# Performance work log

Measured on AMD Instinct MI355X. Metric: run time of the kernel, lower is better.

The kernel has to match this reference:

```python
import jax, jax.numpy as jnp
import numpy as np

B, T, N, L, D, F = 8, 1024, 512, 4096, 512, 64  # batch, target, nodes, leaves, d_model, d_feature
BR = L // N  # branching factor: leaves per node


def setup_inputs() -> dict:
    key = jax.random.key(0)
    ks = jax.random.split(key, 10)
    s = 0.02
    return {
        "root": jax.random.normal(ks[0], (B, 1, F), dtype=jnp.float32),
        "node": jax.random.normal(ks[1], (B, N, D), dtype=jnp.float32),
        "leaf": jax.random.normal(ks[2], (B, L, D), dtype=jnp.float32),
        "target": jax.random.normal(ks[3], (B, T, D), dtype=jnp.float32),
        "Wq": jax.random.normal(ks[4], (D, F), dtype=jnp.float32) * s,
        "bq": jnp.zeros((F,), dtype=jnp.float32),
        "Wk": jax.random.normal(ks[5], (D, F), dtype=jnp.float32) * s,
        "bk": jnp.zeros((F,), dtype=jnp.float32),
        "Wv": jax.random.normal(ks[6], (D, F), dtype=jnp.float32) * s,
        "bv": jnp.zeros((F,), dtype=jnp.float32),
        "Wagg": jax.random.normal(ks[7], (D, 1), dtype=jnp.float32) * s,
        "bagg": jnp.zeros((1,), dtype=jnp.float32),
    }


def reference(root, node, leaf, target, Wq, bq, Wk, bk, Wv, bv, Wagg, bagg):
    # Shared DecoderLinear projections (same weights used for node and leaf).
    q = target @ Wq + bq                      # [B,T,F]
    node_k = node @ Wk + bk                   # [B,N,F]
    node_v = node @ Wv + bv                   # [B,N,F]
    leaf_k = leaf @ Wk + bk                   # [B,L,F]
    leaf_v = leaf @ Wv + bv                   # [B,L,F]

    scale = 1.0 / jnp.sqrt(jnp.asarray(F, dtype=q.dtype))
    # Dual-key attention weights (no value-matmul inside attention()).
    Aqn = jax.nn.softmax(jnp.einsum('btf,bnf->btn', q, node_k) * scale, axis=-1)  # [B,T,N]
    Aql = jax.nn.softmax(jnp.einsum('btf,blf->btl', q, leaf_k) * scale, axis=-1)  # [B,T,L]

    # Tree interpolation: each leaf mixes root, its parent node value, and itself.
    node_rep = jnp.repeat(node_v, BR, axis=1)               # [B,L,F]
    interp = (root + node_rep + leaf_v) / 3.0               # [B,L,F]

    # Upward cumulative aggregation: suffix mean along the leaf dimension.
    rev_cumsum = jnp.cumsum(interp[:, ::-1, :], axis=1)[:, ::-1, :]  # [B,L,F]
    counts = (L - jnp.arange(L)).astype(interp.dtype)[None, :, None]
    upward = rev_cumsum / counts                                     # [B,L,F]

    # Weighted aggregation: learned softmax weights over each node's leaf group.
    w = jax.nn.softmax((leaf @ Wagg + bagg).reshape(B, N, BR), axis=-1)   # [B,N,BR]
    node_hat = jnp.einsum('bnc,bncf->bnf', w, upward.reshape(B, N, BR, F))  # [B,N,F]

    # Fused cat + matmul + softmax.
    A = jnp.concatenate([Aqn, Aql], axis=-1)          # [B,T,N+L]
    V = jnp.concatenate([node_hat, leaf_v], axis=-2)  # [B,N+L,F]
    return jax.nn.softmax(jnp.einsum('btm,bmf->btf', A, V), axis=-1)  # [B,T,F]
```

## Files before the change

kernel.cpp:

```cpp
#include <hip/hip_runtime.h>

#define B_ 8
#define T_ 1024
#define N_ 512
#define L_ 4096
#define D_ 512
#define F_ 64
#define SLICES 8
#define TPS 9
#define KSTR 72
#define XSTR 520

typedef __attribute__((ext_vector_type(8))) short short8;
typedef __attribute__((ext_vector_type(4))) float f32x4;

__device__ __forceinline__ unsigned short f2bf(float x){
    unsigned u = __builtin_bit_cast(unsigned, x);
    u += 0x7FFFu + ((u >> 16) & 1u);
    return (unsigned short)(u >> 16);
}
__device__ __forceinline__ unsigned pack_bf(float lo, float hi){
    return (unsigned)f2bf(lo) | ((unsigned)f2bf(hi) << 16);
}
__device__ __forceinline__ float bf2f(unsigned short s){
    return __builtin_bit_cast(float, ((unsigned)s) << 16);
}
__device__ __forceinline__ short8 frag_from4(unsigned d0, unsigned d1, unsigned d2, unsigned d3){
    union { unsigned u[4]; short8 s; } t;
    t.u[0] = d0; t.u[1] = d1; t.u[2] = d2; t.u[3] = d3;
    return t.s;
}

__global__ __launch_bounds__(64)
void prep_kernel(const float* __restrict__ Wq, const float* __restrict__ bq,
                 const float* __restrict__ Wk, const float* __restrict__ bk,
                 const float* __restrict__ Wv, const float* __restrict__ bv,
                 unsigned short* __restrict__ Wq_t, unsigned short* __restrict__ Wkv_t,
                 float* __restrict__ bq_s, float* __restrict__ bkv)
{
    const int n = blockIdx.x;
    const int lane = threadIdx.x;
    if (n == 192) {
        bq_s[lane]   = bq[lane] * 0.125f;
        bkv[lane]    = bk[lane];
        bkv[64+lane] = bv[lane];
        return;
    }
    const int d0 = lane * 8;
    unsigned short t[8];
    if (n < 64) {
        #pragma unroll
        for (int j = 0; j < 8; ++j) t[j] = f2bf(Wq[(size_t)(d0+j)*F_ + n] * 0.125f);
        *(uint4*)&Wq_t[(size_t)n*D_ + d0] = make_uint4(
            (unsigned)t[0]|((unsigned)t[1]<<16), (unsigned)t[2]|((unsigned)t[3]<<16),
            (unsigned)t[4]|((unsigned)t[5]<<16), (unsigned)t[6]|((unsigned)t[7]<<16));
    } else {
        const int nn  = n - 64;
        const float* W = (nn < 64) ? Wk : Wv;
        const int col = nn & 63;
        #pragma unroll
        for (int j = 0; j < 8; ++j) t[j] = f2bf(W[(size_t)(d0+j)*F_ + col]);
        *(uint4*)&Wkv_t[(size_t)nn*D_ + d0] = make_uint4(
            (unsigned)t[0]|((unsigned)t[1]<<16), (unsigned)t[2]|((unsigned)t[3]<<16),
            (unsigned)t[4]|((unsigned)t[5]<<16), (unsigned)t[6]|((unsigned)t[7]<<16));
    }
}

template<int MODE>
__device__ __forceinline__ void proj_body(
    int r0, unsigned short* Xs, unsigned short* Vt_lds,
    const float* __restrict__ X,
    const unsigned short* __restrict__ Wt,
    const float* __restrict__ bias,
    const float* __restrict__ Wagg, const float* __restrict__ bagg,
    unsigned short* __restrict__ outK, float* __restrict__ outVf,
    unsigned short* __restrict__ outVt, float* __restrict__ outAgg)
{
    constexpr int NPW = (MODE == 0) ? 1 : 2;
    const int tid = threadIdx.x;
    const int w = tid >> 6, l = tid & 63, c = l & 15, h = l >> 4;

    short8 breg[NPW][16];
    #pragma unroll
    for (int p = 0; p < NPW; ++p) {
        const unsigned short* wrow = Wt + (size_t)(16*(NPW*w + p) + c)*D_ + 8*h;
        #pragma unroll
        for (int kk = 0; kk < 16; ++kk)
            breg[p][kk] = *(const short8*)(wrow + kk*32);
    }

    const float4* xsrc = (const float4*)(X + (size_t)r0 * D_);
    #pragma unroll 4
    for (int j = 0; j < 32; ++j) {
        const int s = tid + j * 256;
        const float4 v = xsrc[s];
        *(uint2*)&Xs[(s >> 7)*XSTR + (s & 127)*4] =
            make_uint2(pack_bf(v.x, v.y), pack_bf(v.z, v.w));
    }
    __syncthreads();

    f32x4 acc[NPW][4];
    #pragma unroll
    for (int p = 0; p < NPW; ++p)
        #pragma unroll
        for (int m = 0; m < 4; ++m) acc[p][m] = (f32x4){0,0,0,0};

    #pragma unroll
    for (int kk = 0; kk < 16; ++kk) {
        #pragma unroll
        for (int m = 0; m < 4; ++m) {
            const short8 af = *(const short8*)&Xs[(16*m + c)*XSTR + kk*32 + 8*h];
            #pragma unroll
            for (int p = 0; p < NPW; ++p)
                acc[p][m] = __builtin_amdgcn_mfma_f32_16x16x32_bf16(af, breg[p][kk], acc[p][m], 0,0,0);
        }
    }

    #pragma unroll
    for (int p = 0; p < NPW; ++p) {
        const int s2g = NPW*w + p;
        const float bc = bias[16*s2g + c];
        if (MODE == 0 || s2g < 4) {
            #pragma unroll
            for (int m = 0; m < 4; ++m)
                #pragma unroll
                for (int r = 0; r < 4; ++r)
                    outK[(size_t)(r0 + 16*m + 4*h + r)*F_ + 16*s2g + c] = f2bf(acc[p][m][r] + bc);
        } else if (MODE == 1) {
            #pragma unroll
            for (int m = 0; m < 4; ++m)
                #pragma unroll
                for (int r = 0; r < 4; ++r)
                    outVf[(size_t)(r0 + 16*m + 4*h + r)*F_ + 16*(s2g-4) + c] = acc[p][m][r] + bc;
        } else {
            #pragma unroll
            for (int m = 0; m < 4; ++m)
                #pragma unroll
                for (int r = 0; r < 4; ++r)
                    Vt_lds[(16*(s2g-4) + c)*72 + 16*m + 4*h + r] = f2bf(acc[p][m][r] + bc);
        }
    }

    if constexpr (MODE == 2) {
        {
            const int row = tid >> 2, qd = tid & 3;
            const unsigned short* xr = &Xs[row*XSTR + qd*128];
            const float* wr = Wagg + qd*128;
            float p = 0.f;
            #pragma unroll
            for (int j = 0; j < 16; ++j) {
                const short8 xv = *(const short8*)(xr + j*8);
                const float4 wa0 = *(const float4*)(wr + j*8);
                const float4 wa1 = *(const float4*)(wr + j*8 + 4);
                p += bf2f((unsigned short)xv[0])*wa0.x + bf2f((unsigned short)xv[1])*wa0.y
                   + bf2f((unsigned short)xv[2])*wa0.z + bf2f((unsigned short)xv[3])*wa0.w
                   + bf2f((unsigned short)xv[4])*wa1.x + bf2f((unsigned short)xv[5])*wa1.y
                   + bf2f((unsigned short)xv[6])*wa1.z + bf2f((unsigned short)xv[7])*wa1.w;
            }
            p += __shfl_xor(p, 1);
            p += __shfl_xor(p, 2);
            if (qd == 0) outAgg[r0 + row] = p + bagg[0];
        }
        __syncthreads();
        {
            const int f = tid >> 2, seg = tid & 3;
            const int b = r0 >> 12, l0 = r0 & (L_ - 1);
            const uint4 a0 = *(const uint4*)&Vt_lds[f*72 + seg*16];
            const uint4 a1 = *(const uint4*)&Vt_lds[f*72 + seg*16 + 8];
            unsigned short* dst = outVt + ((size_t)(b*F_ + f))*L_ + l0 + seg*16;
            *(uint4*)dst = a0;
            *(uint4*)(dst + 8) = a1;
        }
    }
}

__global__ __launch_bounds__(256, 2)
void proj_all(const float* __restrict__ target, const float* __restrict__ node,
              const float* __restrict__ leaf,
              const unsigned short* __restrict__ Wq_t,
              const unsigned short* __restrict__ Wkv_t,
              const float* __restrict__ bq_s, const float* __restrict__ bkv,
              const float* __restrict__ Wagg, const float* __restrict__ bagg,
              unsigned short* __restrict__ q_bf, unsigned short* __restrict__ nk_bf,
              float* __restrict__ node_v, unsigned short* __restrict__ lk_bf,
              unsigned short* __restrict__ lvt, float* __restrict__ agg)
{
    __shared__ unsigned short Xs[64 * XSTR];
    __shared__ unsigned short Vt_lds[64 * 72];
    const int blk = blockIdx.x;
    if (blk < 512) {
        proj_body<2>(blk*64, Xs, Vt_lds, leaf, Wkv_t, bkv, Wagg, bagg,
                     lk_bf, nullptr, lvt, agg);
    } else if (blk < 640) {
        proj_body<0>((blk-512)*64, Xs, Vt_lds, target, Wq_t, bq_s, nullptr, nullptr,
                     q_bf, nullptr, nullptr, nullptr);
    } else {
        proj_body<1>((blk-640)*64, Xs, Vt_lds, node, Wkv_t, bkv, nullptr, nullptr,
                     nk_bf, node_v, nullptr, nullptr);
    }
}

__global__ __launch_bounds__(256)
void scan_nh_kernel(const unsigned short* __restrict__ lvt,
                    const float* __restrict__ node_v,
                    const float* __restrict__ root,
                    const float* __restrict__ agg,
                    unsigned short* __restrict__ nh_t)
{
    const int gtid = blockIdx.x * 256 + threadIdx.x;
    const int wv   = gtid >> 6;
    const int lane = threadIdx.x & 63;
    const int b = wv >> 6;
    const int f = wv & 63;

    const unsigned short* vt = lvt + ((size_t)(b*F_ + f))*L_ + lane*64;
    const float rootf = root[b*F_ + f];
    short8 xv[8]; float nv[8]; float gv[8];
    #pragma unroll
    for (int g = 0; g < 8; ++g) {
        xv[g] = *(const short8*)(vt + g*8);
        nv[g] = node_v[((size_t)(b*N_ + lane*8 + g))*F_ + f];
        float s8 = 0.f;
        #pragma unroll
        for (int j = 0; j < 8; ++j) s8 += bf2f((unsigned short)xv[g][j]);
        gv[g] = (s8 + 8.f*(rootf + nv[g])) * (1.f/3.f);
    }

    float s[9];
    s[8] = 0.f;
    #pragma unroll
    for (int j = 7; j >= 0; --j) s[j] = s[j+1] + gv[j];

    float x = s[0];
    const float lsum = x;
    #pragma unroll
    for (int off = 1; off < 64; off <<= 1) {
        float t = __shfl_down(x, off);
        if (lane + off < 64) x += t;
    }
    const float excl = x - lsum;

    const float* aggb = agg + (size_t)b*L_ + lane*64;
    unsigned short out8[8];
    #pragma unroll
    for (int g = 0; g < 8; ++g) {
        const float4 a0 = *(const float4*)(aggb + g*8);
        const float4 a1 = *(const float4*)(aggb + g*8 + 4);
        const float av[8] = {a0.x,a0.y,a0.z,a0.w, a1.x,a1.y,a1.z,a1.w};
        float mx = av[0];
        #pragma unroll
        for (int cc = 1; cc < 8; ++cc) mx = fmaxf(mx, av[cc]);
        float wgt[8]; float wsum = 0.f;
        #pragma unroll
        for (int cc = 0; cc < 8; ++cc) { wgt[cc] = __expf(av[cc] - mx); wsum += wgt[cc]; }

        const float tn = excl + s[g+1];
        float run = 0.f, acc = 0.f;
        #pragma unroll
        for (int cc = 7; cc >= 0; --cc) {
            const int ll = lane*64 + g*8 + cc;
            const float interp = (rootf + nv[g] + bf2f((unsigned short)xv[g][cc])) * (1.f/3.f);
            run += interp;
            const float up = (tn + run) / (float)(L_ - ll);
            acc = fmaf(wgt[cc], up, acc);
        }
        out8[g] = f2bf(acc / wsum);
    }
    *(uint4*)&nh_t[((size_t)(b*F_ + f))*N_ + lane*8] = *(const uint4*)out8;
}

__global__ __launch_bounds__(512, 4)
void attn_kernel(const unsigned short* __restrict__ qb,
                 const unsigned short* __restrict__ nk,
                 const unsigned short* __restrict__ nht,
                 const unsigned short* __restrict__ lk,
                 const unsigned short* __restrict__ lvt,
                 unsigned short* __restrict__ pacc, float* __restrict__ pd)
{
    __shared__ unsigned short Ks[2][64*KSTR];
    __shared__ unsigned short Vt[2][64*KSTR];

    const int wg  = (blockIdx.x & 7) * 64 + (blockIdx.x >> 3);
    const int b   = wg >> 6;
    const int sl  = (wg >> 3) & 7;
    const int t0  = (wg & 7) * 128;

    const int tid = threadIdx.x;
    const int w   = tid >> 6;
    const int l   = tid & 63;
    const int c   = l & 15;
    const int h   = l >> 4;
    const int sm  = tid >> 3;
    const int sc  = tid & 7;

    const unsigned short* qrow = qb + ((size_t)(b*T_ + t0 + w*16 + c))*F_ + 8*h;
    const short8 qf0 = *(const short8*)qrow;
    const short8 qf1 = *(const short8*)(qrow + 32);

    f32x4 accN[4] = {{0,0,0,0},{0,0,0,0},{0,0,0,0},{0,0,0,0}};
    f32x4 accL[4] = {{0,0,0,0},{0,0,0,0},{0,0,0,0},{0,0,0,0}};
    float dsN = 0.f, dsL = 0.f;

    const unsigned short* Knb = nk  + (size_t)b*N_*F_;
    const unsigned short* Klb = lk  + (size_t)b*L_*F_;
    const unsigned short* Vnb = nht + (size_t)b*F_*N_;
    const unsigned short* Vlb = lvt + (size_t)b*F_*L_;

    const int ti0 = sl * TPS;

    uint4 sk0, sv0;
    auto load_tile = [&](int ti) {
        if (ti < 8) {
            sk0 = *(const uint4*)(Knb + (size_t)ti*64*F_ + sm*64 + sc*8);
            sv0 = *(const uint4*)(Vnb + (size_t)sm*N_ + ti*64 + sc*8);
        } else {
            sk0 = *(const uint4*)(Klb + (size_t)(ti-8)*64*F_ + sm*64 + sc*8);
            sv0 = *(const uint4*)(Vlb + (size_t)sm*L_ + (ti-8)*64 + sc*8);
        }
    };
    auto write_tile = [&](int pb) {
        *(uint4*)&Ks[pb][sm*KSTR + sc*8] = sk0;
        *(uint4*)&Vt[pb][sm*KSTR + sc*8] = sv0;
    };

    load_tile(ti0);
    write_tile(0);
    __syncthreads();

    const int srcA = c + 16*((2*h) & 3);
    const int srcB = c + 16*((2*h + 1) & 3);
    const int hs   = h >> 1;

    for (int i = 0; i < TPS; ++i) {
        const int  ti  = ti0 + i;
        const bool isN = ti < 8;
        const int  pb  = i & 1;
        const bool nxt = (i + 1 < TPS);
        if (nxt) load_tile(ti + 1);

        f32x4 st[4] = {{0,0,0,0},{0,0,0,0},{0,0,0,0},{0,0,0,0}};
        #pragma unroll
        for (int ss = 0; ss < 4; ++ss) {
            const short8 kf0 = *(const short8*)&Ks[pb][(16*ss + c)*KSTR + 8*h];
            st[ss] = __builtin_amdgcn_mfma_f32_16x16x32_bf16(kf0, qf0, st[ss], 0,0,0);
            const short8 kf1 = *(const short8*)&Ks[pb][(16*ss + c)*KSTR + 32 + 8*h];
            st[ss] = __builtin_amdgcn_mfma_f32_16x16x32_bf16(kf1, qf1, st[ss], 0,0,0);
        }

        unsigned pk0[4], pk1[4];
        float psum = 0.f;
        #pragma unroll
        for (int ss = 0; ss < 4; ++ss) {
            #pragma unroll
            for (int r = 0; r < 4; ++r) { st[ss][r] = __expf(st[ss][r]); psum += st[ss][r]; }
            pk0[ss] = pack_bf(st[ss][0], st[ss][1]);
            pk1[ss] = pack_bf(st[ss][2], st[ss][3]);
        }
        if (isN) dsN += psum; else dsL += psum;

        #pragma unroll
        for (int k00 = 0; k00 < 2; ++k00) {
            const unsigned d0a = __shfl(pk0[2*k00+0], srcA);
            const unsigned d0b = __shfl(pk0[2*k00+1], srcA);
            const unsigned d1a = __shfl(pk1[2*k00+0], srcA);
            const unsigned d1b = __shfl(pk1[2*k00+1], srcA);
            const unsigned d2a = __shfl(pk0[2*k00+0], srcB);
            const unsigned d2b = __shfl(pk0[2*k00+1], srcB);
            const unsigned d3a = __shfl(pk1[2*k00+0], srcB);
            const unsigned d3b = __shfl(pk1[2*k00+1], srcB);
            const short8 bp = frag_from4(hs ? d0b : d0a, hs ? d1b : d1a,
                                         hs ? d2b : d2a, hs ? d3b : d3a);
            if (isN) {
                #pragma unroll
                for (int s2 = 0; s2 < 4; ++s2) {
                    const short8 af = *(const short8*)&Vt[pb][(16*s2 + c)*KSTR + 32*k00 + 8*h];
                    accN[s2] = __builtin_amdgcn_mfma_f32_16x16x32_bf16(af, bp, accN[s2], 0,0,0);
                }
            } else {
                #pragma unroll
                for (int s2 = 0; s2 < 4; ++s2) {
                    const short8 af = *(const short8*)&Vt[pb][(16*s2 + c)*KSTR + 32*k00 + 8*h];
                    accL[s2] = __builtin_amdgcn_mfma_f32_16x16x32_bf16(af, bp, accL[s2], 0,0,0);
                }
            }
        }

        if (nxt) {
            write_tile(pb ^ 1);
            __syncthreads();
        }
    }

    dsN += __shfl_xor(dsN, 16);  dsN += __shfl_xor(dsN, 32);
    dsL += __shfl_xor(dsL, 16);  dsL += __shfl_xor(dsL, 32);

    const int gt = b*T_ + t0 + w*16 + c;
    unsigned short* baseN = pacc + (((size_t)sl*(B_*T_) + gt)*2 + 0)*F_;
    unsigned short* baseL = baseN + F_;
    #pragma unroll
    for (int s2 = 0; s2 < 4; ++s2) {
        *(unsigned*)&baseN[s2*16 + 4*h]     = pack_bf(accN[s2][0], accN[s2][1]);
        *(unsigned*)&baseN[s2*16 + 4*h + 2] = pack_bf(accN[s2][2], accN[s2][3]);
        *(unsigned*)&baseL[s2*16 + 4*h]     = pack_bf(accL[s2][0], accL[s2][1]);
        *(unsigned*)&baseL[s2*16 + 4*h + 2] = pack_bf(accL[s2][2], accL[s2][3]);
    }
    if (h == 0) {
        pd[((size_t)sl*(B_*T_) + gt)*2 + 0] = dsN;
        pd[((size_t)sl*(B_*T_) + gt)*2 + 1] = dsL;
    }
}

__global__ __launch_bounds__(256)
void combine_kernel(const unsigned short* __restrict__ pacc,
                    const float* __restrict__ pd,
                    float* __restrict__ out)
{
    const int gt = (blockIdx.x * 256 + threadIdx.x) >> 6;
    const int f  = threadIdx.x & 63;

    float aN = 0.f, aL = 0.f, dN = 0.f, dL = 0.f;
    #pragma unroll
    for (int s = 0; s < SLICES; ++s) {
        const size_t base = ((size_t)s*(B_*T_) + gt)*2;
        aN += bf2f(pacc[(base + 0)*F_ + f]);
        aL += bf2f(pacc[(base + 1)*F_ + f]);
        dN += pd[base + 0];
        dL += pd[base + 1];
    }
    float lg = aN / dN + aL / dL;
    float mx = lg;
    #pragma unroll
    for (int off = 1; off < 64; off <<= 1) mx = fmaxf(mx, __shfl_xor(mx, off));
    const float e = __expf(lg - mx);
    float ssum = e;
    #pragma unroll
    for (int off = 1; off < 64; off <<= 1) ssum += __shfl_xor(ssum, off);
    out[(size_t)gt*F_ + f] = e / ssum;
}

extern "C" void kernel_launch(void* const* d_in, const int* in_sizes, int n_in,
                              void* d_out, int out_size, void* d_ws, size_t ws_size,
                              hipStream_t stream)
{
    const float* root   = (const float*)d_in[0];
    const float* node   = (const float*)d_in[1];
    const float* leaf   = (const float*)d_in[2];
    const float* target = (const float*)d_in[3];
    const float* Wq   = (const float*)d_in[4];
    const float* bq   = (const float*)d_in[5];
    const float* Wk   = (const float*)d_in[6];
    const float* bk   = (const float*)d_in[7];
    const float* Wv   = (const float*)d_in[8];
    const float* bv   = (const float*)d_in[9];
    const float* Wagg = (const float*)d_in[10];
    const float* bagg = (const float*)d_in[11];
    float* out = (float*)d_out;

    char* wp = (char*)d_ws;
    unsigned short* q_bf  = (unsigned short*)wp; wp += (size_t)B_*T_*F_*2;
    unsigned short* nk_bf = (unsigned short*)wp; wp += (size_t)B_*N_*F_*2;
    unsigned short* lk_bf = (unsigned short*)wp; wp += (size_t)B_*L_*F_*2;
    unsigned short* lvt   = (unsigned short*)wp; wp += (size_t)B_*F_*L_*2;
    unsigned short* nht   = (unsigned short*)wp; wp += (size_t)B_*F_*N_*2;
    unsigned short* Wq_t  = (unsigned short*)wp; wp += (size_t)64*D_*2;
    unsigned short* Wkv_t = (unsigned short*)wp; wp += (size_t)128*D_*2;
    float* node_v = (float*)wp; wp += (size_t)B_*N_*F_*4;
    float* agg    = (float*)wp; wp += (size_t)B_*L_*4;
    float* bq_s   = (float*)wp; wp += 512;
    float* bkv    = (float*)wp; wp += 512;
    unsigned short* pacc = (unsigned short*)wp; wp += (size_t)SLICES*B_*T_*2*F_*2;
    float* pd     = (float*)wp;

    prep_kernel<<<193, 64, 0, stream>>>(Wq, bq, Wk, bk, Wv, bv, Wq_t, Wkv_t, bq_s, bkv);
    proj_all<<<704, 256, 0, stream>>>(target, node, leaf, Wq_t, Wkv_t, bq_s, bkv,
                                      Wagg, bagg, q_bf, nk_bf, node_v, lk_bf, lvt, agg);
    scan_nh_kernel<<<128, 256, 0, stream>>>(lvt, node_v, root, agg, nht);
    attn_kernel<<<B_*(T_/128)*SLICES, 512, 0, stream>>>(q_bf, nk_bf, nht, lk_bf, lvt, pacc, pd);
    combine_kernel<<<(B_*T_)/4, 256, 0, stream>>>(pacc, pd, out);
}
```

Before: 80.79 us.

## Stage projection weights in LDS instead of holding them in registers

```diff
diff --git a/kernel.cpp b/kernel.cpp
--- a/kernel.cpp
+++ b/kernel.cpp
@@ -68,7 +68,7 @@
 
 template<int MODE>
 __device__ __forceinline__ void proj_body(
-    int r0, unsigned short* Xs, unsigned short* Vt_lds,
+    int r0, unsigned short* Xs, unsigned short* Ws, unsigned short* Vt_lds,
     const float* __restrict__ X,
     const unsigned short* __restrict__ Wt,
     const float* __restrict__ bias,
@@ -76,18 +76,9 @@
     unsigned short* __restrict__ outK, float* __restrict__ outVf,
     unsigned short* __restrict__ outVt, float* __restrict__ outAgg)
 {
-    constexpr int NPW = (MODE == 0) ? 1 : 2;
+    constexpr int NPASS = (MODE == 0) ? 1 : 2;
     const int tid = threadIdx.x;
     const int w = tid >> 6, l = tid & 63, c = l & 15, h = l >> 4;
-
-    short8 breg[NPW][16];
-    #pragma unroll
-    for (int p = 0; p < NPW; ++p) {
-        const unsigned short* wrow = Wt + (size_t)(16*(NPW*w + p) + c)*D_ + 8*h;
-        #pragma unroll
-        for (int kk = 0; kk < 16; ++kk)
-            breg[p][kk] = *(const short8*)(wrow + kk*32);
-    }
 
     const float4* xsrc = (const float4*)(X + (size_t)r0 * D_);
     #pragma unroll 4
@@ -97,51 +88,65 @@
         *(uint2*)&Xs[(s >> 7)*XSTR + (s & 127)*4] =
             make_uint2(pack_bf(v.x, v.y), pack_bf(v.z, v.w));
     }
+    {
+        const int r = tid >> 2, ch = tid & 3;
+        const unsigned short* src = Wt + (size_t)r * D_;
+        #pragma unroll
+        for (int j = 0; j < 16; ++j) {
+            const int u = (ch + 4*j) * 8;
+            *(uint4*)&Ws[r*XSTR + u] = *(const uint4*)(src + u);
+        }
+    }
     __syncthreads();
 
-    f32x4 acc[NPW][4];
-    #pragma unroll
-    for (int p = 0; p < NPW; ++p)
-        #pragma unroll
-        for (int m = 0; m < 4; ++m) acc[p][m] = (f32x4){0,0,0,0};
-
-    #pragma unroll
-    for (int kk = 0; kk < 16; ++kk) {
+    #pragma unroll
+    for (int p = 0; p < NPASS; ++p) {
+        f32x4 acc[4];
+        #pragma unroll
+        for (int m = 0; m < 4; ++m) acc[m] = (f32x4){0,0,0,0};
+
+        #pragma unroll
+        for (int kk = 0; kk < 16; ++kk) {
+            const short8 bfr = *(const short8*)&Ws[(16*w + c)*XSTR + kk*32 + 8*h];
+            #pragma unroll
+            for (int m = 0; m < 4; ++m) {
+                const short8 af = *(const short8*)&Xs[(16*m + c)*XSTR + kk*32 + 8*h];
+                acc[m] = __builtin_amdgcn_mfma_f32_16x16x32_bf16(af, bfr, acc[m], 0,0,0);
+            }
+        }
+
+        const float bc = bias[64*p + 16*w + c];
         #pragma unroll
         for (int m = 0; m < 4; ++m) {
-            const short8 af = *(const short8*)&Xs[(16*m + c)*XSTR + kk*32 + 8*h];
             #pragma unroll
-            for (int p = 0; p < NPW; ++p)
-                acc[p][m] = __builtin_amdgcn_mfma_f32_16x16x32_bf16(af, breg[p][kk], acc[p][m], 0,0,0);
-        }
-    }
-
-    #pragma unroll
-    for (int p = 0; p < NPW; ++p) {
-        const int s2g = NPW*w + p;
-        const float bc = bias[16*s2g + c];
-        if (MODE == 0 || s2g < 4) {
+            for (int r = 0; r < 4; ++r) {
+                const int row = r0 + 16*m + 4*h + r;
+                const float v = acc[m][r] + bc;
+                if (MODE == 0 || p == 0) {
+                    outK[(size_t)row*F_ + 16*w + c] = f2bf(v);
+                } else if (MODE == 1) {
+                    outVf[(size_t)row*F_ + 16*w + c] = v;
+                } else {
+                    Vt_lds[(16*w + c)*72 + 16*m + 4*h + r] = f2bf(v);
+                }
+            }
+        }
+
+        if (p + 1 < NPASS) {
+            __syncthreads();
+            const int r = tid >> 2, ch = tid & 3;
+            const unsigned short* src = Wt + (size_t)(64 + r) * D_;
             #pragma unroll
-            for (int m = 0; m < 4; ++m)
-                #pragma unroll
-                for (int r = 0; r < 4; ++r)
-                    outK[(size_t)(r0 + 16*m + 4*h + r)*F_ + 16*s2g + c] = f2bf(acc[p][m][r] + bc);
-        } else if (MODE == 1) {
-            #pragma unroll
-            for (int m = 0; m < 4; ++m)
-                #pragma unroll
-                for (int r = 0; r < 4; ++r)
-                    outVf[(size_t)(r0 + 16*m + 4*h + r)*F_ + 16*(s2g-4) + c] = acc[p][m][r] + bc;
-        } else {
-            #pragma unroll
-            for (int m = 0; m < 4; ++m)
-                #pragma unroll
-                for (int r = 0; r < 4; ++r)
-                    Vt_lds[(16*(s2g-4) + c)*72 + 16*m + 4*h + r] = f2bf(acc[p][m][r] + bc);
+            for (int j = 0; j < 16; ++j) {
+                const int u = (ch + 4*j) * 8;
+                *(uint4*)&Ws[r*XSTR + u] = *(const uint4*)(src + u);
+            }
+            __syncthreads();
         }
     }
 
     if constexpr (MODE == 2) {
+        __syncthreads();
         {
             const int row = tid >> 2, qd = tid & 3;
             const unsigned short* xr = &Xs[row*XSTR + qd*128];
@@ -161,7 +166,6 @@
             p += __shfl_xor(p, 2);
             if (qd == 0) outAgg[r0 + row] = p + bagg[0];
         }
-        __syncthreads();
         {
             const int f = tid >> 2, seg = tid & 3;
             const int b = r0 >> 12, l0 = r0 & (L_ - 1);
@@ -174,7 +178,7 @@
     }
 }
 
-__global__ __launch_bounds__(256, 2)
+__global__ __launch_bounds__(256)
 void proj_all(const float* __restrict__ target, const float* __restrict__ node,
               const float* __restrict__ leaf,
               const unsigned short* __restrict__ Wq_t,
@@ -186,16 +190,17 @@
               unsigned short* __restrict__ lvt, float* __restrict__ agg)
 {
     __shared__ unsigned short Xs[64 * XSTR];
+    __shared__ unsigned short Ws[64 * XSTR];
     __shared__ unsigned short Vt_lds[64 * 72];
     const int blk = blockIdx.x;
     if (blk < 512) {
-        proj_body<2>(blk*64, Xs, Vt_lds, leaf, Wkv_t, bkv, Wagg, bagg,
+        proj_body<2>(blk*64, Xs, Ws, Vt_lds, leaf, Wkv_t, bkv, Wagg, bagg,
                      lk_bf, nullptr, lvt, agg);
     } else if (blk < 640) {
-        proj_body<0>((blk-512)*64, Xs, Vt_lds, target, Wq_t, bq_s, nullptr, nullptr,
+        proj_body<0>((blk-512)*64, Xs, Ws, Vt_lds, target, Wq_t, bq_s, nullptr, nullptr,
                      q_bf, nullptr, nullptr, nullptr);
     } else {
-        proj_body<1>((blk-640)*64, Xs, Vt_lds, node, Wkv_t, bkv, nullptr, nullptr,
+        proj_body<1>((blk-640)*64, Xs, Ws, Vt_lds, node, Wkv_t, bkv, nullptr, nullptr,
                      nk_bf, node_v, nullptr, nullptr);
     }
 }
```

Result: slower. 86.90 us (+7.6%).

## Restructure projection kernel to 512 threads with streamed weight fragments

Applied to the files above, without the earlier changes.

```diff
diff --git a/kernel.cpp b/kernel.cpp
--- a/kernel.cpp
+++ b/kernel.cpp
@@ -76,79 +76,79 @@
     unsigned short* __restrict__ outK, float* __restrict__ outVf,
     unsigned short* __restrict__ outVt, float* __restrict__ outAgg)
 {
-    constexpr int NPW = (MODE == 0) ? 1 : 2;
+    constexpr int NT = (MODE == 0) ? 2 : 4;
     const int tid = threadIdx.x;
     const int w = tid >> 6, l = tid & 63, c = l & 15, h = l >> 4;
-
-    short8 breg[NPW][16];
-    #pragma unroll
-    for (int p = 0; p < NPW; ++p) {
-        const unsigned short* wrow = Wt + (size_t)(16*(NPW*w + p) + c)*D_ + 8*h;
-        #pragma unroll
-        for (int kk = 0; kk < 16; ++kk)
-            breg[p][kk] = *(const short8*)(wrow + kk*32);
-    }
+    const int m  = w & 3;
+    const int nb = (w >> 2) * NT;
+
+    const unsigned short* wbase = Wt + (size_t)(16*nb + c)*D_ + 8*h;
+    short8 b0[NT], b1[NT];
+    #pragma unroll
+    for (int t = 0; t < NT; ++t) b0[t] = *(const short8*)(wbase + (size_t)t*16*D_);
 
     const float4* xsrc = (const float4*)(X + (size_t)r0 * D_);
-    #pragma unroll 4
-    for (int j = 0; j < 32; ++j) {
-        const int s = tid + j * 256;
+    #pragma unroll
+    for (int j = 0; j < 16; ++j) {
+        const int s = tid + j * 512;
         const float4 v = xsrc[s];
         *(uint2*)&Xs[(s >> 7)*XSTR + (s & 127)*4] =
             make_uint2(pack_bf(v.x, v.y), pack_bf(v.z, v.w));
     }
     __syncthreads();
 
-    f32x4 acc[NPW][4];
-    #pragma unroll
-    for (int p = 0; p < NPW; ++p)
-        #pragma unroll
-        for (int m = 0; m < 4; ++m) acc[p][m] = (f32x4){0,0,0,0};
-
-    #pragma unroll
-    for (int kk = 0; kk < 16; ++kk) {
-        #pragma unroll
-        for (int m = 0; m < 4; ++m) {
-            const short8 af = *(const short8*)&Xs[(16*m + c)*XSTR + kk*32 + 8*h];
+    f32x4 acc[NT];
+    #pragma unroll
+    for (int t = 0; t < NT; ++t) acc[t] = (f32x4){0,0,0,0};
+
+    const unsigned short* arow = &Xs[(16*m + c)*XSTR + 8*h];
+
+    #pragma unroll
+    for (int kk = 0; kk < 16; kk += 2) {
+        #pragma unroll
+        for (int t = 0; t < NT; ++t)
+            b1[t] = *(const short8*)(wbase + (size_t)t*16*D_ + (kk+1)*32);
+        const short8 af0 = *(const short8*)(arow + kk*32);
+        #pragma unroll
+        for (int t = 0; t < NT; ++t)
+            acc[t] = __builtin_amdgcn_mfma_f32_16x16x32_bf16(af0, b0[t], acc[t], 0,0,0);
+        if (kk + 2 < 16) {
             #pragma unroll
-            for (int p = 0; p < NPW; ++p)
-                acc[p][m] = __builtin_amdgcn_mfma_f32_16x16x32_bf16(af, breg[p][kk], acc[p][m], 0,0,0);
-        }
-    }
-
-    #pragma unroll
-    for (int p = 0; p < NPW; ++p) {
-        const int s2g = NPW*w + p;
-        const float bc = bias[16*s2g + c];
-        if (MODE == 0 || s2g < 4) {
-            #pragma unroll
-            for (int m = 0; m < 4; ++m)
-                #pragma unroll
-                for (int r = 0; r < 4; ++r)
-                    outK[(size_t)(r0 + 16*m + 4*h + r)*F_ + 16*s2g + c] = f2bf(acc[p][m][r] + bc);
-        } else if (MODE == 1) {
-            #pragma unroll
-            for (int m = 0; m < 4; ++m)
-                #pragma unroll
-                for (int r = 0; r < 4; ++r)
-                    outVf[(size_t)(r0 + 16*m + 4*h + r)*F_ + 16*(s2g-4) + c] = acc[p][m][r] + bc;
-        } else {
-            #pragma unroll
-            for (int m = 0; m < 4; ++m)
-                #pragma unroll
-                for (int r = 0; r < 4; ++r)
-                    Vt_lds[(16*(s2g-4) + c)*72 + 16*m + 4*h + r] = f2bf(acc[p][m][r] + bc);
+            for (int t = 0; t < NT; ++t)
+                b0[t] = *(const short8*)(wbase + (size_t)t*16*D_ + (kk+2)*32);
+        }
+        const short8 af1 = *(const short8*)(arow + (kk+1)*32);
+        #pragma unroll
+        for (int t = 0; t < NT; ++t)
+            acc[t] = __builtin_amdgcn_mfma_f32_16x16x32_bf16(af1, b1[t], acc[t], 0,0,0);
+    }
+
+    #pragma unroll
+    for (int t = 0; t < NT; ++t) {
+        const int nt = nb + t;
+        const float bc = bias[16*nt + c];
+        #pragma unroll
+        for (int r = 0; r < 4; ++r) {
+            const int row = r0 + 16*m + 4*h + r;
+            const float v = acc[t][r] + bc;
+            if (MODE == 0 || nt < 4) {
+                outK[(size_t)row*F_ + 16*nt + c] = f2bf(v);
+            } else if (MODE == 1) {
+                outVf[(size_t)row*F_ + 16*(nt-4) + c] = v;
+            } else {
+                Vt_lds[(16*(nt-4) + c)*72 + 16*m + 4*h + r] = f2bf(v);
+            }
         }
     }
 
     if constexpr (MODE == 2) {
         {
-            const int row = tid >> 2, qd = tid & 3;
-            const unsigned short* xr = &Xs[row*XSTR + qd*128];
-            const float* wr = Wagg + qd*128;
+            const int row = tid >> 3, qd = tid & 7;
+            const unsigned short* xr = &Xs[row*XSTR + qd*64];
+            const float* wr = Wagg + qd*64;
             float p = 0.f;
             #pragma unroll
-            for (int j = 0; j < 16; ++j) {
+            for (int j = 0; j < 8; ++j) {
                 const short8 xv = *(const short8*)(xr + j*8);
                 const float4 wa0 = *(const float4*)(wr + j*8);
                 const float4 wa1 = *(const float4*)(wr + j*8 + 4);
@@ -159,22 +159,20 @@
             }
             p += __shfl_xor(p, 1);
             p += __shfl_xor(p, 2);
+            p += __shfl_xor(p, 4);
             if (qd == 0) outAgg[r0 + row] = p + bagg[0];
         }
         __syncthreads();
         {
-            const int f = tid >> 2, seg = tid & 3;
+            const int f = tid >> 3, seg = tid & 7;
             const int b = r0 >> 12, l0 = r0 & (L_ - 1);
-            const uint4 a0 = *(const uint4*)&Vt_lds[f*72 + seg*16];
-            const uint4 a1 = *(const uint4*)&Vt_lds[f*72 + seg*16 + 8];
-            unsigned short* dst = outVt + ((size_t)(b*F_ + f))*L_ + l0 + seg*16;
-            *(uint4*)dst = a0;
-            *(uint4*)(dst + 8) = a1;
-        }
-    }
-}
-
-__global__ __launch_bounds__(256, 2)
+            const uint4 a0 = *(const uint4*)&Vt_lds[f*72 + seg*8];
+            *(uint4*)(outVt + ((size_t)(b*F_ + f))*L_ + l0 + seg*8) = a0;
+        }
+    }
+}
+
+__global__ __launch_bounds__(512, 4)
 void proj_all(const float* __restrict__ target, const float* __restrict__ node,
               const float* __restrict__ leaf,
               const unsigned short* __restrict__ Wq_t,
@@ -472,7 +470,7 @@
     float* pd     = (float*)wp;
 
     prep_kernel<<<193, 64, 0, stream>>>(Wq, bq, Wk, bk, Wv, bv, Wq_t, Wkv_t, bq_s, bkv);
-    proj_all<<<704, 256, 0, stream>>>(target, node, leaf, Wq_t, Wkv_t, bq_s, bkv,
+    proj_all<<<704, 512, 0, stream>>>(target, node, leaf, Wq_t, Wkv_t, bq_s, bkv,
                                       Wagg, bagg, q_bf, nk_bf, node_v, lk_bf, lvt, agg);
     scan_nh_kernel<<<128, 256, 0, stream>>>(lvt, node_v, root, agg, nht);
     attn_kernel<<<B_*(T_/128)*SLICES, 512, 0, stream>>>(q_bf, nk_bf, nht, lk_bf, lvt, pacc, pd);
```

Result: slower. 110.4 us (+36.7%).
